# Optimization experiments

Measured on AMD Instinct MI355X. Metric: run time of the kernel, lower is better.

## Reference

```python
import jax, jax.numpy as jnp
import numpy as np

B, S, D_IN = 2, 2048, 1024
D_OUT, HEADS = 1024, 16
HD = D_OUT // HEADS  # head_dim = 64


def rope_sincos(seq_len, head_dim):
    half = head_dim // 2
    inv_freq = 1.0 / (10000.0 ** (jnp.arange(half, dtype=jnp.float32) / half))
    angles = jnp.arange(seq_len, dtype=jnp.float32)[:, None] * inv_freq[None, :]  # (s, hd/2)
    return jnp.sin(angles), jnp.cos(angles)


def apply_rope(x, sin, cos):
    # x: (b, h, s, hd); interleaved-pair rotation as in the torch module
    b, h, s, hd = x.shape
    xp = x.reshape(b, h, s, hd // 2, 2)
    x0, x1 = xp[..., 0], xp[..., 1]
    sin = sin[:s][None, None, :, :]
    cos = cos[:s][None, None, :, :]
    r0 = x0 * cos - x1 * sin
    r1 = x0 * sin + x1 * cos
    return jnp.stack([r0, r1], axis=-1).reshape(b, h, s, hd)


def setup_inputs() -> dict:
    key = jax.random.key(0)
    kx, kq, kk, kv, ko = jax.random.split(key, 5)
    scale = 0.02
    return {
        "x": jax.random.normal(kx, (B, S, D_IN), dtype=jnp.float32),
        "Wq": jax.random.normal(kq, (D_IN, D_OUT), dtype=jnp.float32) * scale,
        "Wk": jax.random.normal(kk, (D_IN, D_OUT), dtype=jnp.float32) * scale,
        "Wv": jax.random.normal(kv, (D_IN, D_OUT), dtype=jnp.float32) * scale,
        "Wo": jax.random.normal(ko, (D_OUT, D_OUT), dtype=jnp.float32) * scale,
    }


def reference(x, Wq, Wk, Wv, Wo):
    b, s, _ = x.shape
    q = (x @ Wq).reshape(b, s, HEADS, HD).transpose(0, 2, 1, 3)  # (b,h,s,hd)
    k = (x @ Wk).reshape(b, s, HEADS, HD).transpose(0, 2, 1, 3)
    v = (x @ Wv).reshape(b, s, HEADS, HD).transpose(0, 2, 1, 3)
    sin, cos = rope_sincos(s, HD)
    q = apply_rope(q, sin, cos)
    k = apply_rope(k, sin, cos)
    scores = jnp.einsum('bhqd,bhkd->bhqk', q, k)
    causal = jnp.triu(jnp.ones((s, s), dtype=bool), 1)
    scores = jnp.where(causal[None, None], -jnp.inf, scores)
    weights = jax.nn.softmax(scores / jnp.sqrt(jnp.float32(HD)), axis=-1)
    ctx = jnp.einsum('bhqk,bhkd->bhqd', weights, v)
    ctx = ctx.transpose(0, 2, 1, 3).reshape(b, s, D_OUT)
    return ctx @ Wo
```

## Files before the change

### kernel.cpp

```cpp
#include <hip/hip_runtime.h>
#include <cstdint>
#include <cstddef>

#define BB 2
#define SS 2048
#define DD 1024
#define HH 16
#define HDD 64

typedef unsigned short u16;
typedef unsigned int u32;
typedef __attribute__((ext_vector_type(8))) short bf16x8;
typedef __attribute__((ext_vector_type(4))) float f32x4;

__device__ __forceinline__ u16 f2bf(float f) {
    union { float f; u32 u; } c; c.f = f;
    u32 r = c.u + 0x7fffu + ((c.u >> 16) & 1u);
    return (u16)(r >> 16);
}
__device__ __forceinline__ void gll16(const void* g, void* l) {
    __builtin_amdgcn_global_load_lds(
        (const __attribute__((address_space(1))) void*)g,
        (__attribute__((address_space(3))) void*)l, 16, 0, 0);
}

__global__ __launch_bounds__(256) void prep_all(
    const float* X, const float* Wq, const float* Wk, const float* Wv, const float* Wo,
    u16* Xb, u16* WTbase)
{
    __shared__ float L[32][33];
    const int z = blockIdx.z;
    if (z < 4) {
        const float* Ws[4] = {Wq, Wk, Wv, Wo};
        const float* W = Ws[z];
        u16* WT = WTbase + (size_t)z * (DD * DD);
        const int k0 = blockIdx.x * 32, n0 = blockIdx.y * 32;
        const int tx = threadIdx.x & 31, ty = threadIdx.x >> 5;
        #pragma unroll
        for (int i = 0; i < 4; i++)
            L[ty + 8 * i][tx] = W[(size_t)(k0 + ty + 8 * i) * DD + n0 + tx];
        __syncthreads();
        #pragma unroll
        for (int i = 0; i < 4; i++) {
            const int n = ty + 8 * i;
            WT[(size_t)(n0 + n) * DD + k0 + tx] = f2bf(L[tx][n]);
        }
    } else {
        const int bid = blockIdx.x + 32 * blockIdx.y;
        const int idx0 = bid * 256 + threadIdx.x;
        #pragma unroll
        for (int i = 0; i < 4; i++) {
            const int c = idx0 + i * 262144;
            const float4 v = *(const float4*)&X[(size_t)c * 4];
            ushort4 o;
            o.x = f2bf(v.x); o.y = f2bf(v.y); o.z = f2bf(v.z); o.w = f2bf(v.w);
            *(ushort4*)&Xb[(size_t)c * 4] = o;
        }
    }
}

__global__ __launch_bounds__(256) void gemm_qkv(
    const u16* __restrict__ Xb, const u16* __restrict__ WTall, u16* __restrict__ QKVb)
{
    __shared__ __align__(16) u16 sm[16384];
    const int tid = threadIdx.x;
    const int lane = tid & 63;
    const int w = tid >> 6;
    const int li = lane & 15, quad = lane >> 4;
    const int wr = w >> 1, wc = w & 1;
    const int which = blockIdx.x >> 3;
    const int n0 = (blockIdx.x & 7) * 128;
    const int m0 = blockIdx.y * 64;
    const u16* BT = WTall + (size_t)which * (DD * DD);
    u16* outp = QKVb + (size_t)which * ((size_t)BB * HH * SS * HDD);
    const float scale = (which == 0) ? 0.125f * 1.4426950408889634f : 1.0f;

    const int arow = tid >> 2;
    const int acol = (tid & 3) * 8;
    const int wbase = (tid >> 6) * 1024;

    auto stage = [&](int t, int buf) {
        char* base = (char*)(sm + buf * 6144);
        const int k0 = t * 32;
        gll16(Xb + (size_t)(m0 + arow) * DD + k0 + acol, base + wbase);
        #pragma unroll
        for (int rr = 0; rr < 2; rr++)
            gll16(BT + (size_t)(n0 + rr * 64 + arow) * DD + k0 + acol,
                  base + 4096 + rr * 4096 + wbase);
    };

    f32x4 acc[2][4] = {};
    stage(0, 0);
    __syncthreads();
    for (int t = 0; t < 32; t++) {
        const int buf = t & 1;
        if (t < 31) stage(t + 1, buf ^ 1);
        const u16* tA = sm + buf * 6144;
        const u16* tB = tA + 2048;
        bf16x8 a[2], b[4];
        #pragma unroll
        for (int f = 0; f < 2; f++)
            a[f] = *(const bf16x8*)(tA + (wr * 32 + f * 16 + li) * 32 + quad * 8);
        #pragma unroll
        for (int f = 0; f < 4; f++)
            b[f] = *(const bf16x8*)(tB + (wc * 64 + f * 16 + li) * 32 + quad * 8);
        #pragma unroll
        for (int fm = 0; fm < 2; fm++)
            #pragma unroll
            for (int fn = 0; fn < 4; fn++)
                acc[fm][fn] = __builtin_amdgcn_mfma_f32_16x16x32_bf16(
                    a[fm], b[fn], acc[fm][fn], 0, 0, 0);
        __syncthreads();
    }

    const int bidx = m0 >> 11;
    const int s0 = m0 & (SS - 1);
    if (which < 2) {
        float* tabc = (float*)(sm + 8192);
        float* tabs = tabc + 2048;
        {
            const int j = tid & 31;
            const int sb = tid >> 5;
            const float inv = exp2f((float)j * -0.4152410118609203f);
            #pragma unroll
            for (int k = 0; k < 8; k++) {
                const int sl = k * 8 + sb;
                float sn, cs;
                sincosf((float)(s0 + sl) * inv, &sn, &cs);
                tabc[sl * 32 + j] = cs;
                tabs[sl * 32 + j] = sn;
            }
        }
        float (*Ts)[128] = (float(*)[128])sm;
        #pragma unroll
        for (int p = 0; p < 2; p++) {
            if (p) __syncthreads();
            if (wr == p) {
                #pragma unroll
                for (int fm = 0; fm < 2; fm++)
                    #pragma unroll
                    for (int fn = 0; fn < 4; fn++)
                        #pragma unroll
                        for (int r = 0; r < 4; r++)
                            Ts[fm * 16 + quad * 4 + r][wc * 64 + fn * 16 + li] = acc[fm][fn][r];
            }
            __syncthreads();
            #pragma unroll
            for (int i = 0; i < 2; i++) {
                const int c = tid + 256 * i;
                const int mr = c >> 4;
                const int nc = c & 15;
                const int sl = p * 32 + mr;
                const int s = s0 + sl;
                const int n = n0 + nc * 8;
                const int h = n >> 6, hd0 = n & 63;
                const int j0 = hd0 >> 1;
                const float4 v0 = *(const float4*)&Ts[mr][nc * 8];
                const float4 v1 = *(const float4*)&Ts[mr][nc * 8 + 4];
                const float4 cs4 = *(const float4*)&tabc[sl * 32 + j0];
                const float4 sn4 = *(const float4*)&tabs[sl * 32 + j0];
                u32 w0, w1, w2, w3;
                w0 = (u32)f2bf((v0.x * cs4.x - v0.y * sn4.x) * scale) |
                     ((u32)f2bf((v0.x * sn4.x + v0.y * cs4.x) * scale) << 16);
                w1 = (u32)f2bf((v0.z * cs4.y - v0.w * sn4.y) * scale) |
                     ((u32)f2bf((v0.z * sn4.y + v0.w * cs4.y) * scale) << 16);
                w2 = (u32)f2bf((v1.x * cs4.z - v1.y * sn4.z) * scale) |
                     ((u32)f2bf((v1.x * sn4.z + v1.y * cs4.z) * scale) << 16);
                w3 = (u32)f2bf((v1.z * cs4.w - v1.w * sn4.w) * scale) |
                     ((u32)f2bf((v1.z * sn4.w + v1.w * cs4.w) * scale) << 16);
                uint4 ov; ov.x = w0; ov.y = w1; ov.z = w2; ov.w = w3;
                *(uint4*)&outp[((size_t)(bidx * HH + h) * SS + s) * HDD + hd0] = ov;
            }
        }
    } else {
        float (*Ts)[64] = (float(*)[64])sm;
        #pragma unroll
        for (int fm = 0; fm < 2; fm++)
            #pragma unroll
            for (int fn = 0; fn < 4; fn++)
                *(float4*)&Ts[wc * 64 + fn * 16 + li][wr * 32 + fm * 16 + quad * 4] =
                    make_float4(acc[fm][fn][0], acc[fm][fn][1],
                                acc[fm][fn][2], acc[fm][fn][3]);
        __syncthreads();
        #pragma unroll
        for (int i = 0; i < 4; i++) {
            const int c = tid + 256 * i;
            const int nr = c >> 3;
            const int mc = c & 7;
            const int n = n0 + nr;
            const int h = n >> 6, hd = n & 63;
            const float4 v0 = *(const float4*)&Ts[nr][mc * 8];
            const float4 v1 = *(const float4*)&Ts[nr][mc * 8 + 4];
            uint4 ov;
            ov.x = (u32)f2bf(v0.x) | ((u32)f2bf(v0.y) << 16);
            ov.y = (u32)f2bf(v0.z) | ((u32)f2bf(v0.w) << 16);
            ov.z = (u32)f2bf(v1.x) | ((u32)f2bf(v1.y) << 16);
            ov.w = (u32)f2bf(v1.z) | ((u32)f2bf(v1.w) << 16);
            *(uint4*)&outp[((size_t)(bidx * HH + h) * HDD + hd) * SS + s0 + mc * 8] = ov;
        }
    }
}

__global__ __launch_bounds__(512) void attn_mfma(
    const u16* __restrict__ Qb, const u16* __restrict__ Kb,
    const u16* __restrict__ Vt, u16* __restrict__ ctxb)
{
    __shared__ u16 Ks[128][72];
    __shared__ u16 Vs[64][136];
    __shared__ u16 Ps[8][16][136];
    const int tid = threadIdx.x;
    const int lane = tid & 63;
    const int w = tid >> 6;
    const int li = lane & 15;
    const int quad = lane >> 4;
    const int bh = blockIdx.x;
    const int i = blockIdx.y;
    const int q0A = 128 * i;
    const int q0B = 128 * (15 - i);
    const int ntA = i + 1;
    const int ntB = 16 - i;

    bf16x8 aQA0, aQA1, aQB0, aQB1;
    {
        const u16* qa = Qb + ((size_t)bh * SS + q0A + 16 * w + li) * HDD + quad * 8;
        aQA0 = *(const bf16x8*)qa;
        aQA1 = *(const bf16x8*)(qa + 32);
        const u16* qb = Qb + ((size_t)bh * SS + q0B + 16 * w + li) * HDD + quad * 8;
        aQB0 = *(const bf16x8*)qb;
        aQB1 = *(const bf16x8*)(qb + 32);
    }

    f32x4 OA[4] = {}, OB[4] = {};
    float lA[4] = {}, lB[4] = {};

    const int kr = tid >> 2;
    const int kc = (tid & 3) * 16;
    const int vr = tid >> 3;
    const int vc = (tid & 7) * 16;

    auto process = [&](const bf16x8& aQ0, const bf16x8& aQ1,
                       f32x4 (&O)[4], float (&l_r)[4], const bool diag) {
        f32x4 S[8];
        __builtin_amdgcn_s_setprio(1);
        #pragma unroll
        for (int t = 0; t < 8; t++) {
            const bf16x8 b0 = *(const bf16x8*)&Ks[16 * t + li][quad * 8];
            const bf16x8 b1 = *(const bf16x8*)&Ks[16 * t + li][32 + quad * 8];
            f32x4 a2 = {};
            a2 = __builtin_amdgcn_mfma_f32_16x16x32_bf16(aQ0, b0, a2, 0, 0, 0);
            a2 = __builtin_amdgcn_mfma_f32_16x16x32_bf16(aQ1, b1, a2, 0, 0, 0);
            S[t] = a2;
        }
        __builtin_amdgcn_s_setprio(0);
        if (diag) {
            #pragma unroll
            for (int t = 0; t < 8; t++)
                #pragma unroll
                for (int r = 0; r < 4; r++)
                    if (16 * t + li > 16 * w + quad * 4 + r) S[t][r] = -1e30f;
        }
        float p[4][8];
        #pragma unroll
        for (int r = 0; r < 4; r++) {
            float ls = 0.f;
            #pragma unroll
            for (int t = 0; t < 8; t++) {
                p[r][t] = exp2f(S[t][r] - 8.0f);
                ls += p[r][t];
            }
            l_r[r] += ls;
        }
        #pragma unroll
        for (int r = 0; r < 4; r++)
            #pragma unroll
            for (int t = 0; t < 8; t++)
                Ps[w][quad * 4 + r][16 * t + li] = f2bf(p[r][t]);
        bf16x8 aP[4];
        #pragma unroll
        for (int c = 0; c < 4; c++)
            aP[c] = *(const bf16x8*)&Ps[w][li][32 * c + quad * 8];
        __builtin_amdgcn_s_setprio(1);
        #pragma unroll
        for (int t2 = 0; t2 < 4; t2++) {
            #pragma unroll
            for (int c = 0; c < 4; c++) {
                const bf16x8 bv = *(const bf16x8*)&Vs[16 * t2 + li][32 * c + quad * 8];
                O[t2] = __builtin_amdgcn_mfma_f32_16x16x32_bf16(aP[c], bv, O[t2], 0, 0, 0);
            }
        }
        __builtin_amdgcn_s_setprio(0);
    };

    for (int jt = 0; jt < ntB; jt++) {
        const int j0 = jt << 7;
        const uint4 k0v = *(const uint4*)(Kb + ((size_t)bh * SS + j0 + kr) * HDD + kc);
        const uint4 k1v = *(const uint4*)(Kb + ((size_t)bh * SS + j0 + kr) * HDD + kc + 8);
        const uint4 v0v = *(const uint4*)(Vt + ((size_t)bh * HDD + vr) * SS + j0 + vc);
        const uint4 v1v = *(const uint4*)(Vt + ((size_t)bh * HDD + vr) * SS + j0 + vc + 8);
        __syncthreads();
        *(uint4*)&Ks[kr][kc] = k0v;
        *(uint4*)&Ks[kr][kc + 8] = k1v;
        *(uint4*)&Vs[vr][vc] = v0v;
        *(uint4*)&Vs[vr][vc + 8] = v1v;
        __syncthreads();

        if (jt < ntA) process(aQA0, aQA1, OA, lA, jt == ntA - 1);
        process(aQB0, aQB1, OB, lB, jt == ntB - 1);
    }

    const int b = bh >> 4, h = bh & 15;
    #pragma unroll
    for (int r = 0; r < 4; r++) {
        float la = lA[r], lb = lB[r];
        #pragma unroll
        for (int off = 1; off < 16; off <<= 1) {
            la += __shfl_xor(la, off);
            lb += __shfl_xor(lb, off);
        }
        const float invA = 1.f / la;
        const float invB = 1.f / lb;
        const int rowA = q0A + 16 * w + quad * 4 + r;
        const int rowB = q0B + 16 * w + quad * 4 + r;
        #pragma unroll
        for (int t2 = 0; t2 < 4; t2++) {
            ctxb[((size_t)b * SS + rowA) * DD + h * HDD + 16 * t2 + li] = f2bf(OA[t2][r] * invA);
            ctxb[((size_t)b * SS + rowB) * DD + h * HDD + 16 * t2 + li] = f2bf(OB[t2][r] * invB);
        }
    }
}

__global__ __launch_bounds__(256) void gemm_out_mfma(
    const u16* __restrict__ Ab, const u16* __restrict__ WoT, float* __restrict__ out)
{
    __shared__ __align__(16) u16 sm[12288];
    const int tid = threadIdx.x;
    const int lane = tid & 63;
    const int w = tid >> 6;
    const int li = lane & 15, quad = lane >> 4;
    const int wr = w >> 1, wc = w & 1;
    const int n0 = blockIdx.x * 128;
    const int m0 = blockIdx.y * 64;

    const int arow = tid >> 2;
    const int acol = (tid & 3) * 8;
    const int wbase = (tid >> 6) * 1024;

    auto stage = [&](int t, int buf) {
        char* base = (char*)(sm + buf * 6144);
        const int k0 = t * 32;
        gll16(Ab + (size_t)(m0 + arow) * DD + k0 + acol, base + wbase);
        #pragma unroll
        for (int rr = 0; rr < 2; rr++)
            gll16(WoT + (size_t)(n0 + rr * 64 + arow) * DD + k0 + acol,
                  base + 4096 + rr * 4096 + wbase);
    };

    f32x4 acc[2][4] = {};
    stage(0, 0);
    __syncthreads();
    for (int t = 0; t < 32; t++) {
        const int buf = t & 1;
        if (t < 31) stage(t + 1, buf ^ 1);
        const u16* tA = sm + buf * 6144;
        const u16* tB = tA + 2048;
        bf16x8 a[2], b[4];
        #pragma unroll
        for (int f = 0; f < 2; f++)
            a[f] = *(const bf16x8*)(tA + (wr * 32 + f * 16 + li) * 32 + quad * 8);
        #pragma unroll
        for (int f = 0; f < 4; f++)
            b[f] = *(const bf16x8*)(tB + (wc * 64 + f * 16 + li) * 32 + quad * 8);
        #pragma unroll
        for (int fm = 0; fm < 2; fm++)
            #pragma unroll
            for (int fn = 0; fn < 4; fn++)
                acc[fm][fn] = __builtin_amdgcn_mfma_f32_16x16x32_bf16(
                    a[fm], b[fn], acc[fm][fn], 0, 0, 0);
        __syncthreads();
    }

    #pragma unroll
    for (int fm = 0; fm < 2; fm++)
        #pragma unroll
        for (int r = 0; r < 4; r++) {
            const size_t mg = (size_t)(m0 + wr * 32 + fm * 16 + quad * 4 + r) * DD;
            #pragma unroll
            for (int fn = 0; fn < 4; fn++)
                out[mg + n0 + wc * 64 + fn * 16 + li] = acc[fm][fn][r];
        }
}

extern "C" void kernel_launch(void* const* d_in, const int* in_sizes, int n_in,
                              void* d_out, int out_size, void* d_ws, size_t ws_size,
                              hipStream_t stream) {
    const float* x  = (const float*)d_in[0];
    const float* Wq = (const float*)d_in[1];
    const float* Wk = (const float*)d_in[2];
    const float* Wv = (const float*)d_in[3];
    const float* Wo = (const float*)d_in[4];
    float* out = (float*)d_out;

    u16* ws16 = (u16*)d_ws;
    const size_t E = 4194304;
    const size_t M = 1048576;
    u16* QKVb = ws16;
    u16* Qb   = QKVb;
    u16* Kb   = QKVb + E;
    u16* Vt   = QKVb + 2 * E;
    u16* Xb   = ws16 + 3 * E;
    u16* ctxb = Xb;
    u16* WTall = ws16 + 4 * E;
    u16* WoT  = WTall + 3 * M;

    hipLaunchKernelGGL(prep_all, dim3(32, 32, 5), dim3(256), 0, stream,
                       x, Wq, Wk, Wv, Wo, Xb, WTall);
    hipLaunchKernelGGL(gemm_qkv, dim3(24, 64), dim3(256), 0, stream, Xb, WTall, QKVb);
    hipLaunchKernelGGL(attn_mfma, dim3(BB * HH, 8), dim3(512), 0, stream,
                       Qb, Kb, Vt, ctxb);
    hipLaunchKernelGGL(gemm_out_mfma, dim3(8, 64), dim3(256), 0, stream, ctxb, WoT, out);
}
```

Baseline: 202.2 us.

## Triple-buffer GEMM LDS staging with explicit vmcnt waits

Both the QKV and output-projection GEMMs move from double to triple-buffered LDS staging, prefetching two k-tiles ahead. Full __syncthreads barriers are replaced with partial s_waitcnt vmcnt(3) plus s_barrier, so one tile's loads can stay in flight across the barrier. The aim is to hide global-load latency behind the MFMA work. The cost is more LDS per block, which may lower occupancy, and correctness now depends on exact vmcnt counting of the global_load_lds ops (3 per stage).

```diff
diff --git a/kernel.cpp b/kernel.cpp
--- a/kernel.cpp
+++ b/kernel.cpp
@@ -62,7 +62,7 @@
 __global__ __launch_bounds__(256) void gemm_qkv(
     const u16* __restrict__ Xb, const u16* __restrict__ WTall, u16* __restrict__ QKVb)
 {
-    __shared__ __align__(16) u16 sm[16384];
+    __shared__ __align__(16) u16 sm[18432];
     const int tid = threadIdx.x;
     const int lane = tid & 63;
     const int w = tid >> 6;
@@ -80,7 +80,7 @@
     const int wbase = (tid >> 6) * 1024;
 
     auto stage = [&](int t, int buf) {
-        char* base = (char*)(sm + buf * 6144);
+        char* base = (char*)sm + buf * 12288;
         const int k0 = t * 32;
         gll16(Xb + (size_t)(m0 + arow) * DD + k0 + acol, base + wbase);
         #pragma unroll
@@ -91,10 +91,12 @@
 
     f32x4 acc[2][4] = {};
     stage(0, 0);
-    __syncthreads();
+    stage(1, 1);
+    asm volatile("s_waitcnt vmcnt(3)" ::: "memory");
+    __builtin_amdgcn_s_barrier();
     for (int t = 0; t < 32; t++) {
-        const int buf = t & 1;
-        if (t < 31) stage(t + 1, buf ^ 1);
+        const int buf = t % 3;
+        if (t < 30) stage(t + 2, (t + 2) % 3);
         const u16* tA = sm + buf * 6144;
         const u16* tB = tA + 2048;
         bf16x8 a[2], b[4];
@@ -110,8 +112,13 @@
             for (int fn = 0; fn < 4; fn++)
                 acc[fm][fn] = __builtin_amdgcn_mfma_f32_16x16x32_bf16(
                     a[fm], b[fn], acc[fm][fn], 0, 0, 0);
-        __syncthreads();
-    }
+        if (t < 31) {
+            if (t < 30) asm volatile("s_waitcnt vmcnt(3)" ::: "memory");
+            else        asm volatile("s_waitcnt vmcnt(0)" ::: "memory");
+            __builtin_amdgcn_s_barrier();
+        }
+    }
+    __syncthreads();
 
     const int bidx = m0 >> 11;
     const int s0 = m0 & (SS - 1);
@@ -332,7 +339,7 @@
 __global__ __launch_bounds__(256) void gemm_out_mfma(
     const u16* __restrict__ Ab, const u16* __restrict__ WoT, float* __restrict__ out)
 {
-    __shared__ __align__(16) u16 sm[12288];
+    __shared__ __align__(16) u16 sm[18432];
     const int tid = threadIdx.x;
     const int lane = tid & 63;
     const int w = tid >> 6;
@@ -346,7 +353,7 @@
     const int wbase = (tid >> 6) * 1024;
 
     auto stage = [&](int t, int buf) {
-        char* base = (char*)(sm + buf * 6144);
+        char* base = (char*)sm + buf * 12288;
         const int k0 = t * 32;
         gll16(Ab + (size_t)(m0 + arow) * DD + k0 + acol, base + wbase);
         #pragma unroll
@@ -357,10 +364,12 @@
 
     f32x4 acc[2][4] = {};
     stage(0, 0);
-    __syncthreads();
+    stage(1, 1);
+    asm volatile("s_waitcnt vmcnt(3)" ::: "memory");
+    __builtin_amdgcn_s_barrier();
     for (int t = 0; t < 32; t++) {
-        const int buf = t & 1;
-        if (t < 31) stage(t + 1, buf ^ 1);
+        const int buf = t % 3;
+        if (t < 30) stage(t + 2, (t + 2) % 3);
         const u16* tA = sm + buf * 6144;
         const u16* tB = tA + 2048;
         bf16x8 a[2], b[4];
@@ -376,7 +385,11 @@
             for (int fn = 0; fn < 4; fn++)
                 acc[fm][fn] = __builtin_amdgcn_mfma_f32_16x16x32_bf16(
                     a[fm], b[fn], acc[fm][fn], 0, 0, 0);
-        __syncthreads();
+        if (t < 31) {
+            if (t < 30) asm volatile("s_waitcnt vmcnt(3)" ::: "memory");
+            else        asm volatile("s_waitcnt vmcnt(0)" ::: "memory");
+            __builtin_amdgcn_s_barrier();
+        }
     }
 
     #pragma unroll
```

New measurement: 193.9 us (median of 2 runs). 4.1% less time.
